# Kernel tuning notes

Hardware: AMD Instinct MI355X
Metric: run time of the kernel (lower is better)

The kernel has to match this reference:

```python
import jax, jax.numpy as jnp
import numpy as np

N = 50000      # nodes
E = 1_600_000  # edges (avg degree 32)
IN, H, OUT, R = 128, 64, 32, 8
NEG_SLOPE = 0.2


def _rgat(x, src, dst, etype, W, q, k, b, n_nodes):
    """PyG RGATConv, defaults: heads=1, dim=1, additive-self-attention,
    across-relation softmax, concat=True, bias=True, dropout=0 (eval)."""
    # per-relation transform of all nodes: [R, N, O] (cheaper than per-edge bmm since 2*deg >> R)
    t = jnp.einsum('ni,rio->rno', x, W)
    xi = t[etype, dst]                      # [E, O] transformed target feats
    xj = t[etype, src]                      # [E, O] transformed source feats
    a = (xi @ q + xj @ k)[:, 0]             # [E] additive attention logits
    a = jnp.where(a >= 0, a, NEG_SLOPE * a)  # leaky_relu
    # segment softmax over incoming edges of each target node (across relations)
    m = jax.ops.segment_max(a, dst, num_segments=n_nodes)
    m = jnp.where(jnp.isfinite(m), m, 0.0)
    ex = jnp.exp(a - m[dst])
    s = jax.ops.segment_sum(ex, dst, num_segments=n_nodes)
    alpha = ex / (s[dst] + 1e-16)
    out = jax.ops.segment_sum(alpha[:, None] * xj, dst, num_segments=n_nodes)
    return out + b


def setup_inputs() -> dict:
    key = jax.random.key(0)
    ks = jax.random.split(key, 24)
    x = jax.random.normal(ks[0], (N, IN), jnp.float32)
    edge_index = jax.random.randint(ks[1], (2, E), 0, N, jnp.int32)
    edge_type = jax.random.randint(ks[2], (E,), 0, R, jnp.int32)

    def glorot(k, shape, fan_in):
        return jax.random.normal(k, shape, jnp.float32) * (1.0 / np.sqrt(fan_in))

    d = dict(x=x, edge_index=edge_index, edge_type=edge_type)
    # conv1: in->hidden, conv_mu / conv_logvar: hidden->hidden
    d['W1'] = glorot(ks[3], (R, IN, H), IN)
    d['q1'] = glorot(ks[4], (H, 1), H)
    d['k1'] = glorot(ks[5], (H, 1), H)
    d['b1'] = jnp.zeros((H,), jnp.float32)
    d['Wmu'] = glorot(ks[6], (R, H, H), H)
    d['qmu'] = glorot(ks[7], (H, 1), H)
    d['kmu'] = glorot(ks[8], (H, 1), H)
    d['bmu'] = jnp.zeros((H,), jnp.float32)
    d['Wlv'] = glorot(ks[9], (R, H, H), H)
    d['qlv'] = glorot(ks[10], (H, 1), H)
    d['klv'] = glorot(ks[11], (H, 1), H)
    d['blv'] = jnp.zeros((H,), jnp.float32)
    d['Wm'] = glorot(ks[12], (H, OUT), H)   # linear_mu (stored [in,out])
    d['bm'] = jnp.zeros((OUT,), jnp.float32)
    d['Wl'] = glorot(ks[13], (H, OUT), H)   # linear_logvar
    d['bl'] = jnp.zeros((OUT,), jnp.float32)
    return d


def reference(x, edge_index, edge_type, W1, q1, k1, b1,
              Wmu, qmu, kmu, bmu, Wlv, qlv, klv, blv, Wm, bm, Wl, bl):
    src, dst = edge_index[0], edge_index[1]
    hidden = jax.nn.relu(_rgat(x, src, dst, edge_type, W1, q1, k1, b1, N))
    mu = jax.nn.relu(_rgat(hidden, src, dst, edge_type, Wmu, qmu, kmu, bmu, N))
    mu = mu @ Wm + bm                       # dropout is identity in eval
    logvar = jax.nn.relu(_rgat(hidden, src, dst, edge_type, Wlv, qlv, klv, blv, N))
    logvar = logvar @ Wl + bl
    logstd = 0.5 * logvar
    return (mu, logstd)
```

## Files before the change

### kernel.cpp

```cpp
#include <hip/hip_runtime.h>
#include <cstdint>

#define HDIM 64
#define ODIM 32
#define NEG_SLOPE 0.2f
#define SCHUNK 2048
#define EPB 8192

typedef __attribute__((ext_vector_type(8))) short v8s;
typedef __attribute__((ext_vector_type(4))) float v4f;

__device__ __forceinline__ unsigned f2bf_rne(float f) {
  unsigned u = __float_as_uint(f);
  return (u + 0x7FFFu + ((u >> 16) & 1u)) >> 16;
}

__device__ __forceinline__ unsigned fenc(float f) {
  unsigned u = __float_as_uint(f);
  return (u & 0x80000000u) ? ~u : (u | 0x80000000u);
}
__device__ __forceinline__ float fdec(unsigned e) {
  unsigned u = (e & 0x80000000u) ? (e ^ 0x80000000u) : ~e;
  return __uint_as_float(u);
}

__global__ __launch_bounds__(256) void cvt_bf16_kernel(
    const float* __restrict__ in, unsigned short* __restrict__ out, int n) {
  int i = (blockIdx.x * 256 + threadIdx.x) * 4;
  if (i + 3 < n) {
    float4 v = *(const float4*)&in[i];
    ushort4 o;
    o.x = (unsigned short)f2bf_rne(v.x);
    o.y = (unsigned short)f2bf_rne(v.y);
    o.z = (unsigned short)f2bf_rne(v.z);
    o.w = (unsigned short)f2bf_rne(v.w);
    *(ushort4*)&out[i] = o;
  }
}

__global__ __launch_bounds__(256) void transpose_w_kernel(
    const float* __restrict__ W1, const float* __restrict__ Wmu,
    const float* __restrict__ Wlv, const float* __restrict__ Wm,
    const float* __restrict__ Wl, unsigned short* __restrict__ W1t,
    unsigned short* __restrict__ Wct, unsigned short* __restrict__ Wlt2) {
  const int b = blockIdx.x;
  if (b < 8) {
    const int r = b;
    for (int idx = threadIdx.x; idx < 128 * 64; idx += 256) {
      const int kk = idx >> 6, o = idx & 63;
      W1t[((size_t)r * 64 + o) * 128 + kk] =
          (unsigned short)f2bf_rne(W1[((size_t)r * 128 + kk) * 64 + o]);
    }
  } else if (b < 24) {
    const int s = (b - 8) >> 3, r = (b - 8) & 7;
    const float* src = s ? Wlv : Wmu;
    for (int idx = threadIdx.x; idx < 64 * 64; idx += 256) {
      const int kk = idx >> 6, o = idx & 63;
      Wct[((size_t)s * 64 + o) * 512 + r * 64 + kk] =
          (unsigned short)f2bf_rne(src[((size_t)r * 64 + kk) * 64 + o]);
    }
  } else {
    const int s = b - 24;
    const float* src = s ? Wl : Wm;
    for (int idx = threadIdx.x; idx < 32 * 64; idx += 256) {
      const int o = idx >> 6, c = idx & 63;
      Wlt2[((size_t)s * 32 + o) * 64 + c] =
          (unsigned short)f2bf_rne(src[(size_t)c * 32 + o]);
    }
  }
}

__global__ __launch_bounds__(256) void prep_T_kernel(
    const float* __restrict__ W1, const float* __restrict__ q1,
    const float* __restrict__ k1, const float* __restrict__ Wmu,
    const float* __restrict__ qmu, const float* __restrict__ kmu,
    const float* __restrict__ Wlv, const float* __restrict__ qlv,
    const float* __restrict__ klv, float* __restrict__ T) {
  if (blockIdx.x == 0) {
    for (int idx = threadIdx.x; idx < 2048; idx += 256) {
      const int j = idx >> 6, c = idx & 63;
      const int isk = j >> 4, sr = j & 15, s = sr >> 3, r = sr & 7;
      const float* W = s ? Wlv : Wmu;
      const float* vec = s ? (isk ? klv : qlv) : (isk ? kmu : qmu);
      float acc = 0.f;
      for (int o = 0; o < 64; o++)
        acc += W[((size_t)r * 64 + c) * 64 + o] * vec[o];
      T[idx] = acc;
    }
  } else {
    for (int idx = threadIdx.x; idx < 2048; idx += 256) {
      const int j = idx >> 7, kk = idx & 127;
      const int isk = j >> 3, r = j & 7;
      const float* vec = isk ? k1 : q1;
      float acc = 0.f;
      for (int c = 0; c < 64; c++)
        acc += W1[((size_t)r * 128 + kk) * 64 + c] * vec[c];
      T[2048 + idx] = acc;
    }
  }
}

__global__ __launch_bounds__(256) void count_deg_kernel(
    const int* __restrict__ dst, const int* __restrict__ etype,
    int* __restrict__ deg, int E) {
  int e = blockIdx.x * 256 + threadIdx.x;
  if (e < E) atomicAdd(&deg[dst[e] * 8 + etype[e]], 1);
}

__global__ __launch_bounds__(256) void scan_p1(const int* __restrict__ deg,
                                               int* __restrict__ bsum, int n) {
  int base = blockIdx.x * SCHUNK + threadIdx.x * 8;
  int s = 0;
#pragma unroll
  for (int j = 0; j < 8; j++) {
    int i = base + j;
    if (i < n) s += deg[i];
  }
#pragma unroll
  for (int d = 1; d < 64; d <<= 1) s += __shfl_xor(s, d, 64);
  __shared__ int ws[4];
  if ((threadIdx.x & 63) == 0) ws[threadIdx.x >> 6] = s;
  __syncthreads();
  if (threadIdx.x == 0) bsum[blockIdx.x] = ws[0] + ws[1] + ws[2] + ws[3];
}

__global__ __launch_bounds__(256) void scan_p2(int* bsum, int nb) {
  __shared__ int wsum[4];
  const int i = threadIdx.x;
  int v = (i < nb) ? bsum[i] : 0;
  const int orig = v;
  const int lane = i & 63, w = i >> 6;
#pragma unroll
  for (int d = 1; d < 64; d <<= 1) {
    int up = __shfl_up(v, d, 64);
    if (lane >= d) v += up;
  }
  if (lane == 63) wsum[w] = v;
  __syncthreads();
  int woff = 0;
#pragma unroll
  for (int k = 0; k < 4; k++) woff += (k < w) ? wsum[k] : 0;
  if (i < nb) bsum[i] = woff + v - orig;
}

__global__ __launch_bounds__(256) void scan_p3(const int* __restrict__ deg,
                                               const int* __restrict__ bsum,
                                               int* __restrict__ row_ptr,
                                               int n) {
  int base = blockIdx.x * SCHUNK + threadIdx.x * 8;
  int vals[8];
  int s = 0;
#pragma unroll
  for (int j = 0; j < 8; j++) {
    int i = base + j;
    vals[j] = (i < n) ? deg[i] : 0;
    s += vals[j];
  }
  int lane = threadIdx.x & 63, w = threadIdx.x >> 6;
  int v = s;
#pragma unroll
  for (int d = 1; d < 64; d <<= 1) {
    int up = __shfl_up(v, d, 64);
    if (lane >= d) v += up;
  }
  __shared__ int wsum[4];
  if (lane == 63) wsum[w] = v;
  __syncthreads();
  int woff = 0;
#pragma unroll
  for (int i = 0; i < 4; i++) woff += (i < w) ? wsum[i] : 0;
  int off = bsum[blockIdx.x] + woff + v - s;
#pragma unroll
  for (int j = 0; j < 8; j++) {
    int i = base + j;
    off += vals[j];
    if (i < n) row_ptr[i + 1] = off;
  }
  if (blockIdx.x == 0 && threadIdx.x == 0) row_ptr[0] = 0;
}

__global__ __launch_bounds__(256) void bucket_cursor_init(
    const int* __restrict__ rp2, int* __restrict__ cursor, int N, int nb) {
  int i = threadIdx.x;
  if (i < nb) cursor[i] = rp2[(size_t)min(i * 256, N) * 8];
}

__global__ __launch_bounds__(256) void bucket_pass1(
    const int* __restrict__ src, const int* __restrict__ dst,
    const int* __restrict__ etype, int* __restrict__ cursor,
    unsigned* __restrict__ tmp, int E) {
  __shared__ int hist[256];
  __shared__ int binstart[256];
  __shared__ int gbase[256];
  __shared__ int fill[256];
  __shared__ int wsum[4];
  __shared__ unsigned stage[EPB];
  __shared__ unsigned char binof[EPB];
  const int tid = threadIdx.x;
  const int e0 = blockIdx.x * EPB;
  const int cnt = min(EPB, E - e0);

  hist[tid] = 0;
  fill[tid] = 0;
  __syncthreads();
  for (int j = tid; j < cnt; j += 256) atomicAdd(&hist[dst[e0 + j] >> 8], 1);
  __syncthreads();

  const int hv = hist[tid];
  {
    const int lane = tid & 63, w = tid >> 6;
    int iv = hv;
#pragma unroll
    for (int d = 1; d < 64; d <<= 1) {
      int up = __shfl_up(iv, d, 64);
      if (lane >= d) iv += up;
    }
    if (lane == 63) wsum[w] = iv;
    __syncthreads();
    int woff = 0;
#pragma unroll
    for (int i = 0; i < 4; i++) woff += (i < w) ? wsum[i] : 0;
    binstart[tid] = woff + iv - hv;
    if (hv > 0) gbase[tid] = atomicAdd(&cursor[tid], hv);
  }
  __syncthreads();

  for (int j = tid; j < cnt; j += 256) {
    const int d = dst[e0 + j];
    const int b = d >> 8;
    const unsigned rec = ((unsigned)(d & 255) << 19) |
                         ((unsigned)etype[e0 + j] << 16) |
                         (unsigned)src[e0 + j];
    const int slot = binstart[b] + atomicAdd(&fill[b], 1);
    stage[slot] = rec;
    binof[slot] = (unsigned char)b;
  }
  __syncthreads();

  for (int s = tid; s < cnt; s += 256) {
    const int b = binof[s];
    tmp[gbase[b] + (s - binstart[b])] = stage[s];
  }
}

__global__ __launch_bounds__(256) void bucket_pass2(
    const int* __restrict__ rp2, const unsigned* __restrict__ tmp,
    int* __restrict__ edges, int N) {
  __shared__ int rp[2049];
  __shared__ int fill[2048];
  const int tid = threadIdx.x;
  const int rowbase = blockIdx.x * 256;
  const int rowcnt = min(256, N - rowbase);
  for (int i = tid; i <= rowcnt * 8; i += 256)
    rp[i] = rp2[(size_t)rowbase * 8 + i];
  for (int i = tid; i < 2048; i += 256) fill[i] = 0;
  __syncthreads();
  const int beg = rp[0];
  const int endv = rp[rowcnt * 8];
  for (int i = beg + tid; i < endv; i += 256) {
    const unsigned rec = tmp[i];
    const int bin = rec >> 16;
    const int pos = rp[bin] + atomicAdd(&fill[bin], 1);
    edges[pos] = (int)(rec & 0x7FFFFu);
  }
}

__global__ __launch_bounds__(256) void transform1_mfma(
    const unsigned short* __restrict__ xb,
    const unsigned short* __restrict__ W1t, unsigned short* __restrict__ tb,
    int N) {
  __shared__ unsigned short st[4][16][72];
  const int r = blockIdx.x;
  const int tid = threadIdx.x;
  const int w = tid >> 6;
  const int lane = tid & 63;
  const int quad = lane >> 4;
  const int mrow = lane & 15;
  const int n0w = blockIdx.y * 64 + w * 16;

  const int gA = min(n0w + mrow, N - 1);
  const unsigned short* arow = xb + (size_t)gA * 128 + quad * 8;
  const unsigned short* wrow = W1t + ((size_t)r * 64 + mrow) * 128 + quad * 8;

  v4f acc[4];
#pragma unroll
  for (int tt = 0; tt < 4; tt++) acc[tt] = (v4f){0.f, 0.f, 0.f, 0.f};

#pragma unroll
  for (int k0 = 0; k0 < 128; k0 += 32) {
    v8s a = *(const v8s*)(arow + k0);
#pragma unroll
    for (int tt = 0; tt < 4; tt++) {
      v8s b = *(const v8s*)(wrow + (size_t)tt * 16 * 128 + k0);
      acc[tt] = __builtin_amdgcn_mfma_f32_16x16x32_bf16(a, b, acc[tt], 0, 0, 0);
    }
  }

#pragma unroll
  for (int i = 0; i < 4; i++)
#pragma unroll
    for (int tt = 0; tt < 4; tt++)
      st[w][quad * 4 + i][tt * 16 + mrow] =
          (unsigned short)f2bf_rne(acc[tt][i]);
  __syncthreads();

  const int row = lane >> 2, cg = lane & 3;
  const int gns = n0w + row;
  if (gns < N) {
    const uint4 v0 = *(const uint4*)&st[w][row][cg * 16];
    const uint4 v1 = *(const uint4*)&st[w][row][cg * 16 + 8];
    uint4* dst = (uint4*)&tb[((size_t)r * N + gns) * 64 + cg * 16];
    dst[0] = v0;
    dst[1] = v1;
  }
}

__global__ __launch_bounds__(256) void logit1_kernel(
    const unsigned short* __restrict__ xb, const float* __restrict__ T1,
    float* __restrict__ aq1, float* __restrict__ ak1,
    unsigned* __restrict__ maxk_enc, int N) {
  __shared__ float Ts[2048];
  __shared__ float wred[4][8];
  for (int i = threadIdx.x; i < 2048; i += 256) Ts[i] = T1[i];
  __syncthreads();
  const int n0 = blockIdx.x * 256 + threadIdx.x;
  const bool valid = n0 < N;
  const int n = valid ? n0 : N - 1;
  const unsigned short* xr = xb + (size_t)n * 128;

  float dq[8], dk[8];
#pragma unroll
  for (int j = 0; j < 8; j++) {
    dq[j] = 0.f;
    dk[j] = 0.f;
  }
  for (int d = 0; d < 16; d++) {
    const uint4 u = *(const uint4*)(xr + d * 8);
    float xv[8];
    xv[0] = __uint_as_float(u.x << 16);
    xv[1] = __uint_as_float(u.x & 0xFFFF0000u);
    xv[2] = __uint_as_float(u.y << 16);
    xv[3] = __uint_as_float(u.y & 0xFFFF0000u);
    xv[4] = __uint_as_float(u.z << 16);
    xv[5] = __uint_as_float(u.z & 0xFFFF0000u);
    xv[6] = __uint_as_float(u.w << 16);
    xv[7] = __uint_as_float(u.w & 0xFFFF0000u);
    const int base = d * 8;
#pragma unroll
    for (int j = 0; j < 8; j++) {
#pragma unroll
      for (int c = 0; c < 8; c++) {
        dq[j] = fmaf(xv[c], Ts[j * 128 + base + c], dq[j]);
        dk[j] = fmaf(xv[c], Ts[(8 + j) * 128 + base + c], dk[j]);
      }
    }
  }

  const int lane = threadIdx.x & 63, w = threadIdx.x >> 6;
#pragma unroll
  for (int j = 0; j < 8; j++) {
    if (valid) {
      aq1[(size_t)j * N + n] = dq[j];
      ak1[(size_t)j * N + n] = dk[j];
    }
    float kmx = dk[j];
#pragma unroll
    for (int d = 1; d < 64; d <<= 1)
      kmx = fmaxf(kmx, __shfl_xor(kmx, d, 64));
    if (lane == 0) wred[w][j] = kmx;
  }
  __syncthreads();
  if (threadIdx.x < 8) {
    const float bm = fmaxf(fmaxf(wred[0][threadIdx.x], wred[1][threadIdx.x]),
                           fmaxf(wred[2][threadIdx.x], wred[3][threadIdx.x]));
    atomicMax(&maxk_enc[threadIdx.x], fenc(bm));
  }
}

__global__ __launch_bounds__(256) void aggregate_kernel(
    const int* __restrict__ rp2, const int* __restrict__ edges,
    const unsigned short* __restrict__ tb, const float* __restrict__ aq,
    const float* __restrict__ ak, const unsigned* __restrict__ maxk_enc,
    const float* __restrict__ bias, unsigned short* __restrict__ hb, int N) {
  const int tid = threadIdx.x;
  const int w = tid >> 6, o = tid & 63;
  int wid = blockIdx.x * 4 + w;
  const bool valid = wid < N;
  if (!valid) wid = N - 1;
  const int beg = rp2[(size_t)wid * 8];
  const int end = valid ? rp2[(size_t)wid * 8 + 8] : beg;
  const int deg = end - beg;

  const float aqw = aq[(size_t)(o & 7) * N + wid];

  float v = aqw + fdec(maxk_enc[o & 7]);
  v = (v >= 0.f) ? v : NEG_SLOPE * v;
#pragma unroll
  for (int d = 1; d < 8; d <<= 1) v = fmaxf(v, __shfl_xor(v, d, 64));
  const float m = __shfl(v, 0, 64);

  const int g = o >> 3;
  const int cl = o & 7;
  float s = 0.f;
  float acc[8];
#pragma unroll
  for (int c = 0; c < 8; c++) acc[c] = 0.f;

  for (int base = 0; base < deg; base += 64) {
    const int j = base + o;
    const int gcount = min(64, deg - base);
    const int packed = edges[beg + min(j, deg - 1)];
    const int src = packed & 0xFFFF;
    const int rr = packed >> 16;
    const int idx = rr * N + src;
    float x = __shfl(aqw, rr, 64) + ak[idx];
    x = (x >= 0.f) ? x : NEG_SLOPE * x;
    const float p = (j < deg) ? __expf(x - m) : 0.f;
    s += p;
    const int g8 = (gcount + 7) & ~7;
    for (int u = 0; u < g8; u += 8) {
      const int e = u + g;
      const float pe = __shfl(p, e, 64);
      const int ie = __shfl(idx, e, 64);
      const uint4 tv = *(const uint4*)(tb + (size_t)ie * 64 + cl * 8);
      const unsigned uu0 = tv.x, uu1 = tv.y, uu2 = tv.z, uu3 = tv.w;
      acc[0] = fmaf(pe, __uint_as_float(uu0 << 16), acc[0]);
      acc[1] = fmaf(pe, __uint_as_float(uu0 & 0xFFFF0000u), acc[1]);
      acc[2] = fmaf(pe, __uint_as_float(uu1 << 16), acc[2]);
      acc[3] = fmaf(pe, __uint_as_float(uu1 & 0xFFFF0000u), acc[3]);
      acc[4] = fmaf(pe, __uint_as_float(uu2 << 16), acc[4]);
      acc[5] = fmaf(pe, __uint_as_float(uu2 & 0xFFFF0000u), acc[5]);
      acc[6] = fmaf(pe, __uint_as_float(uu3 << 16), acc[6]);
      acc[7] = fmaf(pe, __uint_as_float(uu3 & 0xFFFF0000u), acc[7]);
    }
  }
#pragma unroll
  for (int d = 1; d < 64; d <<= 1) s += __shfl_xor(s, d, 64);
#pragma unroll
  for (int d = 8; d < 64; d <<= 1) {
#pragma unroll
    for (int c = 0; c < 8; c++) acc[c] += __shfl_xor(acc[c], d, 64);
  }

  if (valid && g == 0) {
    const float inv = 1.f / (s + 1e-16f);
    unsigned rv[8];
#pragma unroll
    for (int c = 0; c < 8; c++) {
      const float res = acc[c] * inv + bias[cl * 8 + c];
      rv[c] = f2bf_rne(fmaxf(res, 0.f));
    }
    uint4 pkd;
    pkd.x = rv[0] | (rv[1] << 16);
    pkd.y = rv[2] | (rv[3] << 16);
    pkd.z = rv[4] | (rv[5] << 16);
    pkd.w = rv[6] | (rv[7] << 16);
    *(uint4*)(hb + (size_t)wid * 64 + cl * 8) = pkd;
  }
}

__global__ __launch_bounds__(256) void logit2_kernel(
    const unsigned short* __restrict__ hb, const float* __restrict__ T,
    float* __restrict__ aq2, float* __restrict__ ak2,
    unsigned* __restrict__ maxk2_enc, int N) {
  __shared__ float Ts[2048];
  __shared__ float wred[4][16];
  for (int i = threadIdx.x; i < 2048; i += 256) Ts[i] = T[i];
  __syncthreads();
  const int n0 = blockIdx.x * 256 + threadIdx.x;
  const bool valid = n0 < N;
  const int n = valid ? n0 : N - 1;
  float h[64];
  const unsigned short* hr = hb + (size_t)n * 64;
#pragma unroll
  for (int d = 0; d < 8; d++) {
    const uint4 u = *(const uint4*)(hr + d * 8);
    h[d * 8 + 0] = __uint_as_float(u.x << 16);
    h[d * 8 + 1] = __uint_as_float(u.x & 0xFFFF0000u);
    h[d * 8 + 2] = __uint_as_float(u.y << 16);
    h[d * 8 + 3] = __uint_as_float(u.y & 0xFFFF0000u);
    h[d * 8 + 4] = __uint_as_float(u.z << 16);
    h[d * 8 + 5] = __uint_as_float(u.z & 0xFFFF0000u);
    h[d * 8 + 6] = __uint_as_float(u.w << 16);
    h[d * 8 + 7] = __uint_as_float(u.w & 0xFFFF0000u);
  }
  float kmx[16];
#pragma unroll
  for (int j = 0; j < 16; j++) {
    float dq = 0.f, dk = 0.f;
#pragma unroll
    for (int c = 0; c < 64; c++) {
      dq = fmaf(h[c], Ts[j * 64 + c], dq);
      dk = fmaf(h[c], Ts[(16 + j) * 64 + c], dk);
    }
    if (valid) {
      aq2[(size_t)j * N + n] = dq;
      ak2[(size_t)j * N + n] = dk;
    }
    kmx[j] = dk;
  }
  const int lane = threadIdx.x & 63, w = threadIdx.x >> 6;
#pragma unroll
  for (int j = 0; j < 16; j++) {
#pragma unroll
    for (int d = 1; d < 64; d <<= 1)
      kmx[j] = fmaxf(kmx[j], __shfl_xor(kmx[j], d, 64));
    if (lane == 0) wred[w][j] = kmx[j];
  }
  __syncthreads();
  if (threadIdx.x < 16) {
    const float bm = fmaxf(fmaxf(wred[0][threadIdx.x], wred[1][threadIdx.x]),
                           fmaxf(wred[2][threadIdx.x], wred[3][threadIdx.x]));
    atomicMax(&maxk2_enc[threadIdx.x], fenc(bm));
  }
}

__global__ __launch_bounds__(256) void aggregate2g_kernel(
    const int* __restrict__ rp2, const int* __restrict__ edges,
    const unsigned short* __restrict__ hb, const float* __restrict__ aq2,
    const float* __restrict__ ak2, const unsigned* __restrict__ maxk2_enc,
    unsigned* __restrict__ y, float* __restrict__ sbuf, int N) {
  const int tid = threadIdx.x;
  const int w = tid >> 6, o = tid & 63;
  int wid = blockIdx.x * 4 + w;
  const bool valid = wid < N;
  if (!valid) wid = N - 1;

  const float aqw = aq2[(size_t)(o & 15) * N + wid];
  float v = aqw + fdec(maxk2_enc[o & 15]);
  v = (v >= 0.f) ? v : NEG_SLOPE * v;
#pragma unroll
  for (int d = 1; d < 8; d <<= 1) v = fmaxf(v, __shfl_xor(v, d, 64));
  const float m0 = __shfl(v, 0, 64);
  const float m1 = __shfl(v, 8, 64);

  const int grp = o >> 3;
  const int ln = o & 7;
  const float aqr0 = __shfl(aqw, grp, 64);
  const float aqr1 = __shfl(aqw, 8 + grp, 64);

  const int sb = rp2[(size_t)wid * 8 + grp];
  const int se = rp2[(size_t)wid * 8 + grp + 1];

  float acc0[8], acc1[8];
#pragma unroll
  for (int c = 0; c < 8; c++) {
    acc0[c] = 0.f;
    acc1[c] = 0.f;
  }
  float s0 = 0.f, s1 = 0.f;

  const size_t akoff0 = (size_t)grp * N;
  const size_t akoff1 = (size_t)(8 + grp) * N;
  for (int e = sb; e < se; ++e) {
    const int src = edges[e] & 0xFFFF;
    const float akv0 = ak2[akoff0 + src];
    const float akv1 = ak2[akoff1 + src];
    const uint4 hv = *(const uint4*)(hb + (size_t)src * 64 + ln * 8);
    float x0 = aqr0 + akv0;
    float x1 = aqr1 + akv1;
    x0 = (x0 >= 0.f) ? x0 : NEG_SLOPE * x0;
    x1 = (x1 >= 0.f) ? x1 : NEG_SLOPE * x1;
    const float p0 = __expf(x0 - m0);
    const float p1 = __expf(x1 - m1);
    s0 += p0;
    s1 += p1;
    const unsigned uu0 = hv.x, uu1 = hv.y, uu2 = hv.z, uu3 = hv.w;
    const float h0 = __uint_as_float(uu0 << 16);
    const float h1 = __uint_as_float(uu0 & 0xFFFF0000u);
    const float h2 = __uint_as_float(uu1 << 16);
    const float h3 = __uint_as_float(uu1 & 0xFFFF0000u);
    const float h4 = __uint_as_float(uu2 << 16);
    const float h5 = __uint_as_float(uu2 & 0xFFFF0000u);
    const float h6 = __uint_as_float(uu3 << 16);
    const float h7 = __uint_as_float(uu3 & 0xFFFF0000u);
    acc0[0] = fmaf(p0, h0, acc0[0]);
    acc0[1] = fmaf(p0, h1, acc0[1]);
    acc0[2] = fmaf(p0, h2, acc0[2]);
    acc0[3] = fmaf(p0, h3, acc0[3]);
    acc0[4] = fmaf(p0, h4, acc0[4]);
    acc0[5] = fmaf(p0, h5, acc0[5]);
    acc0[6] = fmaf(p0, h6, acc0[6]);
    acc0[7] = fmaf(p0, h7, acc0[7]);
    acc1[0] = fmaf(p1, h0, acc1[0]);
    acc1[1] = fmaf(p1, h1, acc1[1]);
    acc1[2] = fmaf(p1, h2, acc1[2]);
    acc1[3] = fmaf(p1, h3, acc1[3]);
    acc1[4] = fmaf(p1, h4, acc1[4]);
    acc1[5] = fmaf(p1, h5, acc1[5]);
    acc1[6] = fmaf(p1, h6, acc1[6]);
    acc1[7] = fmaf(p1, h7, acc1[7]);
  }

  if (valid) {
    uint4 p0w, p1w;
    p0w.x = f2bf_rne(acc0[0]) | (f2bf_rne(acc0[1]) << 16);
    p0w.y = f2bf_rne(acc0[2]) | (f2bf_rne(acc0[3]) << 16);
    p0w.z = f2bf_rne(acc0[4]) | (f2bf_rne(acc0[5]) << 16);
    p0w.w = f2bf_rne(acc0[6]) | (f2bf_rne(acc0[7]) << 16);
    p1w.x = f2bf_rne(acc1[0]) | (f2bf_rne(acc1[1]) << 16);
    p1w.y = f2bf_rne(acc1[2]) | (f2bf_rne(acc1[3]) << 16);
    p1w.z = f2bf_rne(acc1[4]) | (f2bf_rne(acc1[5]) << 16);
    p1w.w = f2bf_rne(acc1[6]) | (f2bf_rne(acc1[7]) << 16);
    *(uint4*)(y + (size_t)wid * 256 + 4 * o) = p0w;
    *(uint4*)(y + ((size_t)N + wid) * 256 + 4 * o) = p1w;
  }

#pragma unroll
  for (int d = 8; d < 64; d <<= 1) {
    s0 += __shfl_xor(s0, d, 64);
    s1 += __shfl_xor(s1, d, 64);
  }
  if (valid && o == 0) {
    sbuf[(size_t)wid * 2 + 0] = s0;
    sbuf[(size_t)wid * 2 + 1] = s1;
  }
}

__global__ __launch_bounds__(256) void out2_kernel(
    const unsigned short* __restrict__ yb,
    const unsigned short* __restrict__ Wct, const float* __restrict__ sbuf,
    const float* __restrict__ bmu, const float* __restrict__ blv,
    const unsigned short* __restrict__ Wlt2, const float* __restrict__ bm,
    const float* __restrict__ bl, float* __restrict__ out_mu,
    float* __restrict__ out_ls, int N) {
  __shared__ unsigned short hst[64][80];
  const int s = blockIdx.y;
  const int tid = threadIdx.x;
  const int w = tid >> 6, lane = tid & 63;
  const int quad = lane >> 4, mrow = lane & 15;
  const int n0w = blockIdx.x * 64 + w * 16;
  const int gA = min(n0w + mrow, N - 1);
  const unsigned short* arow = yb + ((size_t)s * N + gA) * 512 + quad * 8;
  const unsigned short* wrow = Wct + ((size_t)s * 64 + mrow) * 512 + quad * 8;

  v4f acc[4];
#pragma unroll
  for (int tt = 0; tt < 4; tt++) acc[tt] = (v4f){0.f, 0.f, 0.f, 0.f};
#pragma unroll
  for (int k0 = 0; k0 < 512; k0 += 32) {
    v8s a = *(const v8s*)(arow + k0);
#pragma unroll
    for (int tt = 0; tt < 4; tt++) {
      v8s b = *(const v8s*)(wrow + (size_t)tt * 16 * 512 + k0);
      acc[tt] = __builtin_amdgcn_mfma_f32_16x16x32_bf16(a, b, acc[tt], 0, 0, 0);
    }
  }

  const float* bc = s ? blv : bmu;
#pragma unroll
  for (int i = 0; i < 4; i++) {
    const int node = min(n0w + quad * 4 + i, N - 1);
    const float inv = 1.f / (sbuf[(size_t)node * 2 + s] + 1e-16f);
#pragma unroll
    for (int tt = 0; tt < 4; tt++) {
      hst[w * 16 + quad * 4 + i][tt * 16 + mrow] = (unsigned short)f2bf_rne(
          fmaxf(acc[tt][i] * inv + bc[tt * 16 + mrow], 0.f));
    }
  }
  __syncthreads();

  const unsigned short* ar2 = &hst[w * 16 + mrow][quad * 8];
  v4f acc2[2];
  acc2[0] = (v4f){0.f, 0.f, 0.f, 0.f};
  acc2[1] = (v4f){0.f, 0.f, 0.f, 0.f};
#pragma unroll
  for (int st2 = 0; st2 < 2; st2++) {
    v8s a2 = *(const v8s*)(ar2 + st2 * 32);
#pragma unroll
    for (int t2 = 0; t2 < 2; t2++) {
      v8s b2v = *(const v8s*)(Wlt2 + ((size_t)s * 32 + t2 * 16 + mrow) * 64 +
                              quad * 8 + st2 * 32);
      acc2[t2] =
          __builtin_amdgcn_mfma_f32_16x16x32_bf16(a2, b2v, acc2[t2], 0, 0, 0);
    }
  }

  const float* b2 = s ? bl : bm;
  const float mul = s ? 0.5f : 1.f;
  float* outp = s ? out_ls : out_mu;
#pragma unroll
  for (int t2 = 0; t2 < 2; t2++) {
    const float bo = b2[t2 * 16 + mrow];
#pragma unroll
    for (int i = 0; i < 4; i++) {
      const int node = n0w + quad * 4 + i;
      if (node < N)
        outp[(size_t)node * 32 + t2 * 16 + mrow] = (acc2[t2][i] + bo) * mul;
    }
  }
}

extern "C" void kernel_launch(void* const* d_in, const int* in_sizes, int n_in,
                              void* d_out, int out_size, void* d_ws,
                              size_t ws_size, hipStream_t stream) {
  const float* x = (const float*)d_in[0];
  const int* edge_index = (const int*)d_in[1];
  const int* edge_type = (const int*)d_in[2];
  const float* W1 = (const float*)d_in[3];
  const float* q1 = (const float*)d_in[4];
  const float* k1 = (const float*)d_in[5];
  const float* b1 = (const float*)d_in[6];
  const float* Wmu = (const float*)d_in[7];
  const float* qmu = (const float*)d_in[8];
  const float* kmu = (const float*)d_in[9];
  const float* bmu = (const float*)d_in[10];
  const float* Wlv = (const float*)d_in[11];
  const float* qlv = (const float*)d_in[12];
  const float* klv = (const float*)d_in[13];
  const float* blv = (const float*)d_in[14];
  const float* Wm = (const float*)d_in[15];
  const float* bm = (const float*)d_in[16];
  const float* Wl = (const float*)d_in[17];
  const float* bl = (const float*)d_in[18];

  const int N = in_sizes[0] / 128;
  const int E = in_sizes[2];
  const int R = in_sizes[3] / (128 * 64);

  float* out_mu = (float*)d_out;
  float* out_ls = (float*)d_out + (size_t)N * ODIM;

  char* wsp = (char*)d_ws;
  size_t off = 0;
  auto carve = [&](size_t bytes) {
    void* p = wsp + off;
    off += (bytes + 255) & ~(size_t)255;
    return p;
  };

  void* tbuf = carve((size_t)R * N * 64 * sizeof(unsigned));
  unsigned short* t1b = (unsigned short*)tbuf;
  unsigned short* yb = (unsigned short*)tbuf;
  unsigned* yw = (unsigned*)tbuf;
  unsigned short* xb = (unsigned short*)carve((size_t)N * 128 * 2);
  unsigned short* hb = (unsigned short*)carve((size_t)N * 64 * 2);
  unsigned short* W1t = (unsigned short*)carve((size_t)R * 64 * 128 * 2);
  unsigned short* Wct = (unsigned short*)carve((size_t)2 * 64 * 512 * 2);
  unsigned short* Wlt2 = (unsigned short*)carve((size_t)2 * 32 * 64 * 2);
  float* Tdir = (float*)carve((size_t)4096 * sizeof(float));
  float* aq2 = (float*)carve((size_t)2 * R * N * sizeof(float));
  float* ak2 = (float*)carve((size_t)2 * R * N * sizeof(float));
  unsigned* maxk_enc = (unsigned*)carve(32 * sizeof(unsigned));
  float* sbuf = (float*)carve((size_t)N * 2 * sizeof(float));
  int* deg = (int*)carve((size_t)N * 8 * sizeof(int));
  int* rp2 = (int*)carve(((size_t)N * 8 + 1) * sizeof(int));
  int* bsum = (int*)carve(256 * sizeof(int));
  int* cursor = (int*)carve(256 * sizeof(int));
  unsigned* tmp = (unsigned*)carve((size_t)E * sizeof(unsigned));
  int* edges = (int*)carve((size_t)E * sizeof(int));

  const int* e_src = edge_index;
  const int* e_dst = edge_index + E;

  cvt_bf16_kernel<<<(N * 128 / 4 + 255) / 256, 256, 0, stream>>>(x, xb,
                                                                 N * 128);
  transpose_w_kernel<<<26, 256, 0, stream>>>(W1, Wmu, Wlv, Wm, Wl, W1t, Wct,
                                             Wlt2);
  prep_T_kernel<<<2, 256, 0, stream>>>(W1, q1, k1, Wmu, qmu, kmu, Wlv, qlv,
                                       klv, Tdir);

  hipMemsetAsync(deg, 0, (size_t)N * 8 * sizeof(int), stream);
  hipMemsetAsync(maxk_enc, 0, 32 * sizeof(unsigned), stream);
  count_deg_kernel<<<(E + 255) / 256, 256, 0, stream>>>(e_dst, edge_type, deg,
                                                        E);
  const int n2 = N * 8;
  const int nchunk = (n2 + SCHUNK - 1) / SCHUNK;
  scan_p1<<<nchunk, 256, 0, stream>>>(deg, bsum, n2);
  scan_p2<<<1, 256, 0, stream>>>(bsum, nchunk);
  scan_p3<<<nchunk, 256, 0, stream>>>(deg, bsum, rp2, n2);

  const int nbuck = (N + 255) >> 8;
  bucket_cursor_init<<<1, 256, 0, stream>>>(rp2, cursor, N, nbuck);
  bucket_pass1<<<(E + EPB - 1) / EPB, 256, 0, stream>>>(e_src, e_dst,
                                                        edge_type, cursor,
                                                        tmp, E);
  bucket_pass2<<<nbuck, 256, 0, stream>>>(rp2, tmp, edges, N);

  const int nb64 = (N + 63) / 64;
  const int agg_blocks = (N + 3) / 4;

  transform1_mfma<<<dim3(R, nb64), 256, 0, stream>>>(xb, W1t, t1b, N);
  logit1_kernel<<<(N + 255) / 256, 256, 0, stream>>>(xb, Tdir + 2048, aq2,
                                                     ak2, maxk_enc, N);
  aggregate_kernel<<<agg_blocks, 256, 0, stream>>>(rp2, edges, t1b, aq2, ak2,
                                                   maxk_enc, b1, hb, N);

  logit2_kernel<<<(N + 255) / 256, 256, 0, stream>>>(hb, Tdir, aq2, ak2,
                                                     maxk_enc + 8, N);
  aggregate2g_kernel<<<agg_blocks, 256, 0, stream>>>(
      rp2, edges, hb, aq2, ak2, maxk_enc + 8, yw, sbuf, N);
  out2_kernel<<<dim3(nb64, 2), 256, 0, stream>>>(yb, Wct, sbuf, bmu, blv,
                                                 Wlt2, bm, bl, out_mu, out_ls,
                                                 N);
}
```

Baseline: 550.9 us.

## Fuse second-layer aggregation with output projection MFMA kernel via shared memory

Merges aggregate2g and out2 into one kernel. Each 512-thread block aggregates 8 nodes, keeps the bf16 per-relation aggregates and softmax denominators in LDS, and then runs both MFMA projections in the same block. This removes the global write and read of the large y buffer (N×2×512 bf16) and of sbuf, plus one launch. The cost is MFMA tiles that are only half used (16 rows carry 8 nodes per branch), more LDS use and block syncs, and lower occupancy from the larger blocks.

New measurement: 574.3 us. +4.2%, slower.

```diff
diff --git a/kernel.cpp b/kernel.cpp
--- a/kernel.cpp
+++ b/kernel.cpp
@@ -515,14 +515,21 @@
   }
 }
 
-__global__ __launch_bounds__(256) void aggregate2g_kernel(
+__global__ __launch_bounds__(512) void aggregate2f_kernel(
     const int* __restrict__ rp2, const int* __restrict__ edges,
     const unsigned short* __restrict__ hb, const float* __restrict__ aq2,
     const float* __restrict__ ak2, const unsigned* __restrict__ maxk2_enc,
-    unsigned* __restrict__ y, float* __restrict__ sbuf, int N) {
+    const unsigned short* __restrict__ Wct,
+    const unsigned short* __restrict__ Wlt2, const float* __restrict__ bmu,
+    const float* __restrict__ blv, const float* __restrict__ bm,
+    const float* __restrict__ bl, float* __restrict__ out_mu,
+    float* __restrict__ out_ls, int N) {
+  __shared__ unsigned short ylds[16][520];
+  __shared__ unsigned short hid[16][88];
+  __shared__ float sred[2][8];
   const int tid = threadIdx.x;
   const int w = tid >> 6, o = tid & 63;
-  int wid = blockIdx.x * 4 + w;
+  int wid = blockIdx.x * 8 + w;
   const bool valid = wid < N;
   if (!valid) wid = N - 1;
 
@@ -592,7 +599,7 @@
     acc1[7] = fmaf(p1, h7, acc1[7]);
   }
 
-  if (valid) {
+  {
     uint4 p0w, p1w;
     p0w.x = f2bf_rne(acc0[0]) | (f2bf_rne(acc0[1]) << 16);
     p0w.y = f2bf_rne(acc0[2]) | (f2bf_rne(acc0[3]) << 16);
@@ -602,91 +609,75 @@
     p1w.y = f2bf_rne(acc1[2]) | (f2bf_rne(acc1[3]) << 16);
     p1w.z = f2bf_rne(acc1[4]) | (f2bf_rne(acc1[5]) << 16);
     p1w.w = f2bf_rne(acc1[6]) | (f2bf_rne(acc1[7]) << 16);
-    *(uint4*)(y + (size_t)wid * 256 + 4 * o) = p0w;
-    *(uint4*)(y + ((size_t)N + wid) * 256 + 4 * o) = p1w;
-  }
-
+    *(uint4*)&ylds[w][o * 8] = p0w;
+    *(uint4*)&ylds[8 + w][o * 8] = p1w;
+  }
 #pragma unroll
   for (int d = 8; d < 64; d <<= 1) {
     s0 += __shfl_xor(s0, d, 64);
     s1 += __shfl_xor(s1, d, 64);
   }
-  if (valid && o == 0) {
-    sbuf[(size_t)wid * 2 + 0] = s0;
-    sbuf[(size_t)wid * 2 + 1] = s1;
-  }
-}
-
-__global__ __launch_bounds__(256) void out2_kernel(
-    const unsigned short* __restrict__ yb,
-    const unsigned short* __restrict__ Wct, const float* __restrict__ sbuf,
-    const float* __restrict__ bmu, const float* __restrict__ blv,
-    const unsigned short* __restrict__ Wlt2, const float* __restrict__ bm,
-    const float* __restrict__ bl, float* __restrict__ out_mu,
-    float* __restrict__ out_ls, int N) {
-  __shared__ unsigned short hst[64][80];
-  const int s = blockIdx.y;
-  const int tid = threadIdx.x;
-  const int w = tid >> 6, lane = tid & 63;
-  const int quad = lane >> 4, mrow = lane & 15;
-  const int n0w = blockIdx.x * 64 + w * 16;
-  const int gA = min(n0w + mrow, N - 1);
-  const unsigned short* arow = yb + ((size_t)s * N + gA) * 512 + quad * 8;
-  const unsigned short* wrow = Wct + ((size_t)s * 64 + mrow) * 512 + quad * 8;
-
-  v4f acc[4];
-#pragma unroll
-  for (int tt = 0; tt < 4; tt++) acc[tt] = (v4f){0.f, 0.f, 0.f, 0.f};
-#pragma unroll
-  for (int k0 = 0; k0 < 512; k0 += 32) {
-    v8s a = *(const v8s*)(arow + k0);
-#pragma unroll
-    for (int tt = 0; tt < 4; tt++) {
-      v8s b = *(const v8s*)(wrow + (size_t)tt * 16 * 512 + k0);
-      acc[tt] = __builtin_amdgcn_mfma_f32_16x16x32_bf16(a, b, acc[tt], 0, 0, 0);
-    }
-  }
-
-  const float* bc = s ? blv : bmu;
+  if (o == 0) {
+    sred[0][w] = s0;
+    sred[1][w] = s1;
+  }
+  __syncthreads();
+
+  const int quad = o >> 4, mrow = o & 15;
+  const int ct = w & 3, s = w >> 2;
+  const unsigned short* wrow =
+      Wct + ((size_t)s * 64 + ct * 16 + mrow) * 512 + quad * 8;
+  v4f acc = (v4f){0.f, 0.f, 0.f, 0.f};
+#pragma unroll
+  for (int kk = 0; kk < 16; kk++) {
+    v8s a = *(const v8s*)&ylds[mrow][kk * 32 + quad * 8];
+    v8s b = *(const v8s*)(wrow + kk * 32);
+    acc = __builtin_amdgcn_mfma_f32_16x16x32_bf16(a, b, acc, 0, 0, 0);
+  }
+  const float bch = (s ? blv : bmu)[ct * 16 + mrow];
 #pragma unroll
   for (int i = 0; i < 4; i++) {
-    const int node = min(n0w + quad * 4 + i, N - 1);
-    const float inv = 1.f / (sbuf[(size_t)node * 2 + s] + 1e-16f);
-#pragma unroll
-    for (int tt = 0; tt < 4; tt++) {
-      hst[w * 16 + quad * 4 + i][tt * 16 + mrow] = (unsigned short)f2bf_rne(
-          fmaxf(acc[tt][i] * inv + bc[tt * 16 + mrow], 0.f));
-    }
-  }
-  __syncthreads();
-
-  const unsigned short* ar2 = &hst[w * 16 + mrow][quad * 8];
-  v4f acc2[2];
-  acc2[0] = (v4f){0.f, 0.f, 0.f, 0.f};
-  acc2[1] = (v4f){0.f, 0.f, 0.f, 0.f};
-#pragma unroll
-  for (int st2 = 0; st2 < 2; st2++) {
-    v8s a2 = *(const v8s*)(ar2 + st2 * 32);
+    const int row = quad * 4 + i;
+    if ((row < 8) == (s == 0)) {
+      const float inv = 1.f / (sred[s][row & 7] + 1e-16f);
+      hid[row][ct * 16 + mrow] =
+          (unsigned short)f2bf_rne(fmaxf(acc[i] * inv + bch, 0.f));
+    }
+  }
+  __syncthreads();
+
+  if (w < 2) {
+    const int s2 = w;
+    v4f a2c[2];
+    a2c[0] = (v4f){0.f, 0.f, 0.f, 0.f};
+    a2c[1] = (v4f){0.f, 0.f, 0.f, 0.f};
+#pragma unroll
+    for (int kk = 0; kk < 2; kk++) {
+      v8s a2 = *(const v8s*)&hid[mrow][kk * 32 + quad * 8];
+#pragma unroll
+      for (int t2 = 0; t2 < 2; t2++) {
+        v8s b2 = *(const v8s*)(Wlt2 + ((size_t)s2 * 32 + t2 * 16 + mrow) * 64 +
+                               kk * 32 + quad * 8);
+        a2c[t2] = __builtin_amdgcn_mfma_f32_16x16x32_bf16(a2, b2, a2c[t2], 0,
+                                                          0, 0);
+      }
+    }
+    const float* b2v = s2 ? bl : bm;
+    const float mul = s2 ? 0.5f : 1.f;
+    float* outp = s2 ? out_ls : out_mu;
 #pragma unroll
     for (int t2 = 0; t2 < 2; t2++) {
-      v8s b2v = *(const v8s*)(Wlt2 + ((size_t)s * 32 + t2 * 16 + mrow) * 64 +
-                              quad * 8 + st2 * 32);
-      acc2[t2] =
-          __builtin_amdgcn_mfma_f32_16x16x32_bf16(a2, b2v, acc2[t2], 0, 0, 0);
-    }
-  }
-
-  const float* b2 = s ? bl : bm;
-  const float mul = s ? 0.5f : 1.f;
-  float* outp = s ? out_ls : out_mu;
-#pragma unroll
-  for (int t2 = 0; t2 < 2; t2++) {
-    const float bo = b2[t2 * 16 + mrow];
-#pragma unroll
-    for (int i = 0; i < 4; i++) {
-      const int node = n0w + quad * 4 + i;
-      if (node < N)
-        outp[(size_t)node * 32 + t2 * 16 + mrow] = (acc2[t2][i] + bo) * mul;
+      const float bo = b2v[t2 * 16 + mrow];
+#pragma unroll
+      for (int i = 0; i < 4; i++) {
+        const int row = quad * 4 + i;
+        if ((row < 8) == (s2 == 0)) {
+          const int node = blockIdx.x * 8 + (row & 7);
+          if (node < N)
+            outp[(size_t)node * 32 + t2 * 16 + mrow] =
+                (a2c[t2][i] + bo) * mul;
+        }
+      }
     }
   }
 }
@@ -731,8 +722,6 @@
 
   void* tbuf = carve((size_t)R * N * 64 * sizeof(unsigned));
   unsigned short* t1b = (unsigned short*)tbuf;
-  unsigned short* yb = (unsigned short*)tbuf;
-  unsigned* yw = (unsigned*)tbuf;
   unsigned short* xb = (unsigned short*)carve((size_t)N * 128 * 2);
   unsigned short* hb = (unsigned short*)carve((size_t)N * 64 * 2);
   unsigned short* W1t = (unsigned short*)carve((size_t)R * 64 * 128 * 2);
@@ -742,7 +731,6 @@
   float* aq2 = (float*)carve((size_t)2 * R * N * sizeof(float));
   float* ak2 = (float*)carve((size_t)2 * R * N * sizeof(float));
   unsigned* maxk_enc = (unsigned*)carve(32 * sizeof(unsigned));
-  float* sbuf = (float*)carve((size_t)N * 2 * sizeof(float));
   int* deg = (int*)carve((size_t)N * 8 * sizeof(int));
   int* rp2 = (int*)carve(((size_t)N * 8 + 1) * sizeof(int));
   int* bsum = (int*)carve(256 * sizeof(int));
@@ -778,19 +766,16 @@
   bucket_pass2<<<nbuck, 256, 0, stream>>>(rp2, tmp, edges, N);
 
   const int nb64 = (N + 63) / 64;
-  const int agg_blocks = (N + 3) / 4;
 
   transform1_mfma<<<dim3(R, nb64), 256, 0, stream>>>(xb, W1t, t1b, N);
   logit1_kernel<<<(N + 255) / 256, 256, 0, stream>>>(xb, Tdir + 2048, aq2,
                                                      ak2, maxk_enc, N);
-  aggregate_kernel<<<agg_blocks, 256, 0, stream>>>(rp2, edges, t1b, aq2, ak2,
-                                                   maxk_enc, b1, hb, N);
+  aggregate_kernel<<<(N + 3) / 4, 256, 0, stream>>>(rp2, edges, t1b, aq2, ak2,
+                                                    maxk_enc, b1, hb, N);
 
   logit2_kernel<<<(N + 255) / 256, 256, 0, stream>>>(hb, Tdir, aq2, ak2,
                                                      maxk_enc + 8, N);
-  aggregate2g_kernel<<<agg_blocks, 256, 0, stream>>>(
-      rp2, edges, hb, aq2, ak2, maxk_enc + 8, yw, sbuf, N);
-  out2_kernel<<<dim3(nb64, 2), 256, 0, stream>>>(yb, Wct, sbuf, bmu, blv,
-                                                 Wlt2, bm, bl, out_mu, out_ls,
-                                                 N);
-}
+  aggregate2f_kernel<<<(N + 7) / 8, 512, 0, stream>>>(
+      rp2, edges, hb, aq2, ak2, maxk_enc + 8, Wct, Wlt2, bmu, blv, bm, bl,
+      out_mu, out_ls, N);
+}
```
